# Optimization experiments

Measured on AMD Instinct MI355X. Metric: run time of the kernel, lower is better.

The kernel has to match this reference:

```python
import jax, jax.numpy as jnp
import numpy as np

L = 16            # clip_len
STRIDES = (2, 2)
RADII = (0.15, 0.3)
NSAMPLES = (16, 32)
EPS = 1e-5
NEG_SLOPE = 0.2


def _fps(xyz, npoint):
    # furthest point sampling, xyz: (N, 3) -> (npoint,) int32 indices, start at 0
    N = xyz.shape[0]
    def step(carry, _):
        mind, last = carry
        d = jnp.sum((xyz - xyz[last]) ** 2, axis=-1)
        mind = jnp.minimum(mind, d)
        nxt = jnp.argmax(mind).astype(jnp.int32)
        return (mind, nxt), nxt
    _, rest = jax.lax.scan(step, (jnp.full((N,), 1e10, xyz.dtype), jnp.int32(0)), None, length=npoint - 1)
    return jnp.concatenate([jnp.zeros((1,), jnp.int32), rest])


def _shift_point(xyz, batch, N):
    # torch.roll(points, -1, dims=1) over the temporal axis, with last-frame extrapolation fix
    p = xyz.reshape(batch // L, L, N, 3)
    s = jnp.roll(p, -1, axis=1)
    shift_mean = jnp.mean(s[:, :-1] - p[:, :-1], axis=1)   # (Bc, N, 3)
    s = s.at[:, -1].set(p[:, -1] + shift_mean)
    return s.reshape(batch, N, 3)


def _conv_bn_lrelu(x, w, g, b):
    # 1x1 Conv2d (no bias) + GroupBN (per-channel over all other dims) + LeakyReLU(0.2)
    y = jnp.einsum('oc,bcnk->bonk', w, x)
    mu = jnp.mean(y, axis=(0, 2, 3), keepdims=True)
    var = jnp.var(y, axis=(0, 2, 3), keepdims=True)
    y = (y - mu) * jax.lax.rsqrt(var + EPS) * g[None, :, None, None] + b[None, :, None, None]
    return jnp.where(y > 0, y, NEG_SLOPE * y)


def _sa_module(xyz, features, stride, radius, nsample, layers):
    # xyz: (B, N, 3), features: (B, C, N)
    batch, N = xyz.shape[0], xyz.shape[1]
    q = _shift_point(xyz, batch, N)
    npoint = N // stride if stride > 1 else N
    if stride > 1:
        idx = jax.vmap(lambda p: _fps(p, npoint))(jax.lax.stop_gradient(q))  # (B, npoint)
        q = jax.vmap(lambda p, ix: p[ix])(q, idx)                            # (B, npoint, 3)
    # ball query: first `nsample` neighbors of each query within `radius`, padded with first hit
    d2 = jnp.sum((q[:, :, None, :] - xyz[:, None, :, :]) ** 2, axis=-1)      # (B, npoint, N)
    mask = d2 < radius * radius
    cand = jnp.where(mask, jnp.arange(N, dtype=jnp.int32)[None, None, :], N)
    srt = jnp.sort(cand, axis=-1)[..., :nsample]
    first = srt[..., :1]
    gidx = jnp.where(srt == N, first, srt)
    gidx = jnp.where(gidx == N, 0, gidx)                                     # fallback: no neighbor
    grouped_xyz = jax.vmap(lambda pts, ix: pts[ix])(xyz, gidx)               # (B, npoint, ns, 3)
    dp = (grouped_xyz - q[:, :, None, :]) / radius                           # normalize_dp
    dist = jnp.linalg.norm(dp, axis=-1)                                      # (B, npoint, ns) -> 4th grouped channel
    feats = jnp.swapaxes(features, 1, 2)                                     # (B, N, C)
    grouped_f = jax.vmap(lambda f, ix: f[ix])(feats, gidx)                   # (B, npoint, ns, C)
    x = jnp.concatenate([dp, grouped_f], axis=-1)                            # (B, npoint, ns, 3 + C)
    x = jnp.transpose(x, (0, 3, 1, 2))                                       # (B, 3 + C, npoint, ns)
    for (w, g, b) in layers:
        x = _conv_bn_lrelu(x, w, g, b)
    gate = jax.nn.sigmoid(dist)[:, None, :, :]                               # sigmoid(points[:, -1:])
    out = jnp.max(gate * x, axis=-1)                                         # (B, Cout, npoint)
    return q, out


def _forward(xyz, w1a, g1a, b1a, w1b, g1b, b1b, w2a, g2a, b2a, w2b, g2b, b2b):
    features = jnp.swapaxes(xyz, 1, 2)                                       # features default = xyz^T
    q1, f1 = _sa_module(xyz, features, STRIDES[0], RADII[0], NSAMPLES[0],
                        [(w1a, g1a, b1a), (w1b, g1b, b1b)])
    q2, f2 = _sa_module(q1, f1, STRIDES[1], RADII[1], NSAMPLES[1],
                        [(w2a, g2a, b2a), (w2b, g2b, b2b)])
    return f2                                                                # (32, 256, 128)


def setup_inputs() -> dict:
    key = jax.random.key(0)
    ks = jax.random.split(key, 5)
    B, N = 32, 512   # B = 2 clips * clip_len 16
    xyz = jax.random.uniform(ks[0], (B, N, 3), jnp.float32)
    def w(k, o, i):
        return jax.random.normal(k, (o, i), jnp.float32) / np.sqrt(i).astype(np.float32)
    return {
        'xyz': xyz,
        'w1a': w(ks[1], 64, 6),    'g1a': jnp.ones(64),  'b1a': jnp.zeros(64),
        'w1b': w(ks[2], 128, 64),  'g1b': jnp.ones(128), 'b1b': jnp.zeros(128),
        'w2a': w(ks[3], 128, 131), 'g2a': jnp.ones(128), 'b2a': jnp.zeros(128),
        'w2b': w(ks[4], 256, 128), 'g2b': jnp.ones(256), 'b2b': jnp.zeros(256),
    }


def reference(xyz, w1a, g1a, b1a, w1b, g1b, b1b, w2a, g2a, b2a, w2b, g2b, b2b):
    return _forward(xyz, w1a, g1a, b1a, w1b, g1b, b1b, w2a, g2a, b2a, w2b, g2b, b2b)
```

## Files before the change

### kernel.cpp

```cpp
#include <hip/hip_runtime.h>
#include <hip/hip_bf16.h>
#include <math.h>


#define BATCH 32
#define MCOLS 131072
#define CGRID 2048

typedef __attribute__((ext_vector_type(8))) short short8;
typedef __attribute__((ext_vector_type(4))) short short4v;
typedef __attribute__((ext_vector_type(4))) float f32x4;

__device__ __forceinline__ float b2f(short s) {
    return __uint_as_float(((unsigned)(unsigned short)s) << 16);
}
__device__ __forceinline__ short f2b(float f) {
    __hip_bfloat16 h = __float2bfloat16(f);
    return (short)__builtin_bit_cast(unsigned short, h);
}
__device__ __forceinline__ float dpp_row16_sum(float v) {
    int x;
    x = __builtin_amdgcn_update_dpp(0, __float_as_int(v), 0x111, 0xf, 0xf, true);
    v += __int_as_float(x);
    x = __builtin_amdgcn_update_dpp(0, __float_as_int(v), 0x112, 0xf, 0xf, true);
    v += __int_as_float(x);
    x = __builtin_amdgcn_update_dpp(0, __float_as_int(v), 0x114, 0xf, 0xf, true);
    v += __int_as_float(x);
    x = __builtin_amdgcn_update_dpp(0, __float_as_int(v), 0x118, 0xf, 0xf, true);
    v += __int_as_float(x);
    return v;
}
template<int C>
__device__ __forceinline__ float dpp_max(float v) {
    int x = __builtin_amdgcn_update_dpp(0, __float_as_int(v), C, 0xf, 0xf, true);
    return fmaxf(v, __int_as_float(x));
}
__device__ __forceinline__ float readlane_f(float v, int lane) {
    return __int_as_float(__builtin_amdgcn_readlane(__float_as_int(v), lane));
}

__device__ __forceinline__ void prep_elem(const float* __restrict__ w, int O, int C,
                                          int CK, short* __restrict__ hi,
                                          short* __restrict__ lo, int t) {
    if (t >= O * CK) return;
    int o = t / CK, c = t % CK;
    float f = (c < C) ? w[o * C + c] : 0.f;
    short h = f2b(f);
    float fh = b2f(h);
    int NT = O >> 4;
    int ot = o >> 4, l15 = o & 15;
    int kc = c >> 5, quad = (c & 31) >> 3, j = c & 7;
    size_t idx = (((size_t)kc * NT + ot) * 64 + quad * 16 + l15) * 8 + j;
    hi[idx] = h;
    lo[idx] = f2b(f - fh);
}

__device__ __forceinline__ void shift_elem(const float* __restrict__ xyz,
                                           float* __restrict__ qout, int t, int N) {
    int c = t % 3;
    int n = (t / 3) % N;
    int b = t / (3 * N);
    int l = b & 15;
    float v;
    if (l < 15) {
        v = xyz[((size_t)(b + 1) * N + n) * 3 + c];
    } else {
        int g0 = b - 15;
        float acc = 0.f;
        for (int i = 0; i < 15; ++i) {
            float d = __fsub_rn(xyz[((size_t)(g0 + i + 1) * N + n) * 3 + c],
                                xyz[((size_t)(g0 + i) * N + n) * 3 + c]);
            acc = __fadd_rn(acc, d);
        }
        v = __fadd_rn(xyz[((size_t)b * N + n) * 3 + c], __fdiv_rn(acc, 15.f));
    }
    qout[t] = v;
}

__global__ __launch_bounds__(256) void setup_kernel(
        const float* __restrict__ w1a, const float* __restrict__ w1b,
        const float* __restrict__ w2a, const float* __restrict__ w2b,
        const float* __restrict__ xyz, float* __restrict__ qs1,
        short* w1aH, short* w1aL, short* w1bH, short* w1bL,
        short* w2aH, short* w2aL, short* w2bH, short* w2bL) {
    int bid = blockIdx.x;
    int tid = threadIdx.x;
    if (bid < 8)        prep_elem(w1a, 64, 6, 32,    w1aH, w1aL, bid * 256 + tid);
    else if (bid < 40)  prep_elem(w1b, 128, 64, 64,  w1bH, w1bL, (bid - 8) * 256 + tid);
    else if (bid < 120) prep_elem(w2a, 128, 131, 160, w2aH, w2aL, (bid - 40) * 256 + tid);
    else if (bid < 248) prep_elem(w2b, 256, 128, 128, w2bH, w2bL, (bid - 120) * 256 + tid);
    else {
        int t = (bid - 248) * 256 + tid;
        if (t < BATCH * 512 * 3) shift_elem(xyz, qs1, t, 512);
    }
}

template<int N, int NPOINT>
__device__ __forceinline__ void fps_spine(const float4* __restrict__ qp,
                                          int* __restrict__ sel, int lane) {
    constexpr int P = N / 64;
    float px[P], py[P], pz[P], mind[P];
#pragma unroll
    for (int p = 0; p < P; ++p) {
        float4 v = qp[lane * P + p];
        px[p] = v.x; py[p] = v.y; pz[p] = v.z;
        mind[p] = 1e10f;
    }
    float4 L0 = qp[0];
    float lx = L0.x, ly = L0.y, lz = L0.z;
    for (int s = 1; s < NPOINT; ++s) {
        float mn[P];
#pragma unroll
        for (int p = 0; p < P; ++p) {
            float dx = __fsub_rn(px[p], lx);
            float dy = __fsub_rn(py[p], ly);
            float dz = __fsub_rn(pz[p], lz);
            float d = __fadd_rn(__fadd_rn(__fmul_rn(dx, dx), __fmul_rn(dy, dy)),
                                __fmul_rn(dz, dz));
            float m2 = fminf(mind[p], d);
            mind[p] = m2;
            mn[p] = m2;
        }
        float t[P];
#pragma unroll
        for (int p = 0; p < P; ++p) t[p] = mn[p];
#pragma unroll
        for (int w = P / 2; w >= 1; w >>= 1)
#pragma unroll
            for (int p = 0; p < w; ++p) t[p] = fmaxf(t[p], t[p + w]);
        float local = t[0];
        float m = local;
        m = dpp_max<0x111>(m);
        m = dpp_max<0x112>(m);
        m = dpp_max<0x114>(m);
        m = dpp_max<0x118>(m);
        m = dpp_max<0x142>(m);
        m = dpp_max<0x143>(m);
        float maxd = readlane_f(m, 63);
        int enc = P - 1;
        float bx = px[P - 1], by = py[P - 1], bz = pz[P - 1];
#pragma unroll
        for (int p = P - 2; p >= 0; --p) {
            bool e = (mn[p] == local);
            enc = e ? p : enc;
            bx = e ? px[p] : bx;
            by = e ? py[p] : by;
            bz = e ? pz[p] : bz;
        }
        unsigned long long msk = __ballot(local == maxd);
        int winner = (int)__builtin_ctzll(msk);
        int last = winner * P + __builtin_amdgcn_readlane(enc, winner);
        lx = readlane_f(bx, winner);
        ly = readlane_f(by, winner);
        lz = readlane_f(bz, winner);
        if (lane == 0) sel[s] = last;
    }
}

template<int N, int NPOINT>
__global__ __launch_bounds__(64) void fps_kernel(const float* __restrict__ q,
                                                 float* __restrict__ qsel) {
    int b = blockIdx.x;
    int lane = threadIdx.x;
    __shared__ float4 qp[N];
    __shared__ int sel[NPOINT];
    const float* qb = q + (size_t)b * N * 3;
    for (int j = lane; j < N; j += 64)
        qp[j] = make_float4(qb[j * 3 + 0], qb[j * 3 + 1], qb[j * 3 + 2], 0.f);
    if (lane == 0) sel[0] = 0;
    __syncthreads();
    fps_spine<N, NPOINT>(qp, sel, lane);
    __syncthreads();
    for (int i = lane; i < NPOINT; i += 64) {
        float4 Pt = qp[sel[i]];
        size_t o = ((size_t)b * NPOINT + i) * 3;
        qsel[o + 0] = Pt.x;
        qsel[o + 1] = Pt.y;
        qsel[o + 2] = Pt.z;
    }
}

__device__ void fps256_body(const float* __restrict__ q, float* __restrict__ qsel,
                            int b, char* smem) {
    constexpr int N = 256, NPOINT = 128;
    float4* qp = (float4*)smem;
    int* sel = (int*)(smem + N * 16);
    int tid = threadIdx.x;
    const float* qb = q + (size_t)b * N * 3;
    for (int j = tid; j < N; j += 256)
        qp[j] = make_float4(qb[j * 3 + 0], qb[j * 3 + 1], qb[j * 3 + 2], 0.f);
    if (tid == 0) sel[0] = 0;
    __syncthreads();
    if (tid < 64) fps_spine<N, NPOINT>(qp, sel, tid);
    __syncthreads();
    for (int i = tid; i < NPOINT; i += 256) {
        float4 Pt = qp[sel[i]];
        size_t o = ((size_t)b * NPOINT + i) * 3;
        qsel[o + 0] = Pt.x;
        qsel[o + 1] = Pt.y;
        qsel[o + 2] = Pt.z;
    }
}

template<int N, int NPOINT, int NS, int CF, int CK>
__global__ __launch_bounds__(256) void ballq_kernel(
        const float* __restrict__ xyz,
        const float* __restrict__ qpts,
        const float* __restrict__ feats,
        float r2, float radius,
        short* __restrict__ X, float* __restrict__ gate) {
    static_assert((NS & (NS - 1)) == 0, "NS pow2");
    static_assert(CK % 8 == 0, "CK mult of 8");
    int lane = threadIdx.x & 63;
    int wib = threadIdx.x >> 6;
    int wid = blockIdx.x * 4 + wib;
    int b = wid / NPOINT;
    int i = wid % NPOINT;
    const float* qp = qpts + ((size_t)b * NPOINT + i) * 3;
    float qx = qp[0], qy = qp[1], qz = qp[2];
    __shared__ int gsh[4][NS];
    int* gidx = gsh[wib];
    int taken = 0, first = 0;
    bool any = false;
#pragma unroll
    for (int base = 0; base < N; base += 64) {
        int j = base + lane;
        const float* p = xyz + ((size_t)b * N + j) * 3;
        float dx = __fsub_rn(qx, p[0]);
        float dy = __fsub_rn(qy, p[1]);
        float dz = __fsub_rn(qz, p[2]);
        float d2 = __fadd_rn(__fadd_rn(__fmul_rn(dx, dx), __fmul_rn(dy, dy)),
                             __fmul_rn(dz, dz));
        bool in = d2 < r2;
        unsigned long long mk = __ballot(in);
        if (!any && mk) { first = base + __builtin_ctzll(mk); any = true; }
        int cb = __builtin_popcountll(mk & ((1ull << lane) - 1ull));
        int slot = taken + cb;
        if (in && slot < NS) gidx[slot] = j;
        taken += (int)__builtin_popcountll(mk);
    }
    if (taken < NS) {
        for (int s = taken + lane; s < NS; s += 64) gidx[s] = any ? first : 0;
    }
    __syncthreads();
    int m0 = (b * NPOINT + i) * NS;
    if (lane < NS) {
        int g = gidx[lane];
        const float* p = xyz + ((size_t)b * N + g) * 3;
        float dx = (p[0] - qx) / radius;
        float dy = (p[1] - qy) / radius;
        float dz = (p[2] - qz) / radius;
        float dist = sqrtf(dx * dx + dy * dy + dz * dz);
        gate[m0 + lane] = 1.f / (1.f + expf(-dist));
    }
    for (int e8 = lane * 8; e8 < NS * CK; e8 += 64 * 8) {
        int s = e8 / CK;
        int c0 = e8 % CK;
        int g = gidx[s];
        const float* frow = feats + (size_t)(b * N + g) * CF;
        const float* prow = xyz + ((size_t)b * N + g) * 3;
        short8 v8;
#pragma unroll
        for (int ii = 0; ii < 8; ++ii) {
            int c = c0 + ii;
            float v;
            if (c < 3) {
                float qc = (c == 0) ? qx : ((c == 1) ? qy : qz);
                v = (prow[c] - qc) / radius;
            } else if (c < 3 + CF) {
                v = frow[c - 3];
            } else {
                v = 0.f;
            }
            v8[ii] = f2b(v);
        }
        *(short8*)(X + (size_t)(m0 + s) * CK + c0) = v8;
    }
}

template<int CK, int O, bool AFF, bool FUSE>
__global__ __launch_bounds__(256, 3) void mfma_conv(
        const short* __restrict__ X, const short* __restrict__ Whi,
        const short* __restrict__ Wlo, const float* __restrict__ ss,
        short* __restrict__ Y, float* __restrict__ pS, float* __restrict__ pS2,
        const float* __restrict__ qs2, float* __restrict__ q2c) {
    constexpr int KC = CK / 32;
    constexpr int NT = O / 16;
    constexpr int OW = NT / 4;
    constexpr int LR = CK + 8;
    constexpr int CB = CK / 8;
    __shared__ __align__(16) short xs[64 * LR];
    __shared__ __align__(16) short wh[NT * 512];
    __shared__ __align__(16) short wl[NT * 512];
    __shared__ float ssl[AFF ? 2 * CK : 2];
    __shared__ float sblk[O], s2blk[O];
    static_assert(!FUSE || 64 * LR * 2 >= 256 * 16 + 128 * 4, "fps LDS fits in xs");
    if constexpr (FUSE) {
        if (blockIdx.x >= CGRID) {
            fps256_body(qs2, q2c, (int)blockIdx.x - CGRID, (char*)xs);
            return;
        }
    }
    int tid = threadIdx.x;
    int m0 = blockIdx.x * 64;

    if constexpr (AFF) {
        for (int i = tid; i < 2 * CK; i += 256) ssl[i] = ss[i];
        __syncthreads();
    }
    for (int idx = tid; idx < 64 * CB; idx += 256) {
        int r = idx / CB;
        int col = (idx % CB) * 8;
        short8 v = *(const short8*)(X + (size_t)(m0 + r) * CK + col);
        if constexpr (AFF) {
#pragma unroll
            for (int i = 0; i < 8; ++i) {
                float f = b2f(v[i]);
                f = fmaf(f, ssl[col + i], ssl[CK + col + i]);
                f = f > 0.f ? f : 0.2f * f;
                v[i] = f2b(f);
            }
        }
        *(short8*)(xs + r * LR + col) = v;
    }

    int lane = tid & 63;
    int wave = tid >> 6;
    int l15 = lane & 15;
    int quad = lane >> 4;
    int obase = wave * OW * 16;

    f32x4 acc[4][OW];
#pragma unroll
    for (int mt = 0; mt < 4; ++mt)
#pragma unroll
        for (int ot = 0; ot < OW; ++ot) acc[mt][ot] = (f32x4){0.f, 0.f, 0.f, 0.f};

    for (int kc = 0; kc < KC; ++kc) {
        __syncthreads();
        {
            const short8* gH = (const short8*)Whi + (size_t)kc * NT * 64;
            const short8* gL = (const short8*)Wlo + (size_t)kc * NT * 64;
            short8* lH = (short8*)wh;
            short8* lL = (short8*)wl;
            for (int i = tid; i < NT * 64; i += 256) { lH[i] = gH[i]; lL[i] = gL[i]; }
        }
        __syncthreads();
        short8 bf[4];
#pragma unroll
        for (int mt = 0; mt < 4; ++mt)
            bf[mt] = *(const short8*)(xs + (mt * 16 + l15) * LR + kc * 32 + quad * 8);
#pragma unroll
        for (int ot = 0; ot < OW; ++ot) {
            short8 ah = ((const short8*)wh)[(wave * OW + ot) * 64 + lane];
            short8 al = ((const short8*)wl)[(wave * OW + ot) * 64 + lane];
#pragma unroll
            for (int mt = 0; mt < 4; ++mt) {
                acc[mt][ot] = __builtin_amdgcn_mfma_f32_16x16x32_bf16(ah, bf[mt], acc[mt][ot], 0, 0, 0);
                acc[mt][ot] = __builtin_amdgcn_mfma_f32_16x16x32_bf16(al, bf[mt], acc[mt][ot], 0, 0, 0);
            }
        }
    }

#pragma unroll
    for (int mt = 0; mt < 4; ++mt) {
        size_t ybase = (size_t)(m0 + mt * 16 + l15) * O + obase + quad * 4;
#pragma unroll
        for (int ot = 0; ot < OW; ++ot) {
            short4v pk;
#pragma unroll
            for (int r4 = 0; r4 < 4; ++r4) pk[r4] = f2b(acc[mt][ot][r4]);
            *(short4v*)(Y + ybase + ot * 16) = pk;
        }
    }
#pragma unroll
    for (int ot = 0; ot < OW; ++ot) {
#pragma unroll
        for (int r4 = 0; r4 < 4; ++r4) {
            float s = 0.f, s2 = 0.f;
#pragma unroll
            for (int mt = 0; mt < 4; ++mt) {
                float v = acc[mt][ot][r4];
                s += v;
                s2 = fmaf(v, v, s2);
            }
            s = dpp_row16_sum(s);
            s2 = dpp_row16_sum(s2);
            if (l15 == 15) {
                int o = obase + ot * 16 + quad * 4 + r4;
                sblk[o] = s;
                s2blk[o] = s2;
            }
        }
    }
    __syncthreads();
    for (int o = tid; o < O; o += 256) {
        pS [(size_t)o * CGRID + blockIdx.x] = sblk[o];
        pS2[(size_t)o * CGRID + blockIdx.x] = s2blk[o];
    }
}

template<int O>
__global__ __launch_bounds__(256) void stats_fin(
        const float* __restrict__ pS, const float* __restrict__ pS2,
        const float* __restrict__ gm, const float* __restrict__ bt,
        float* __restrict__ norm) {
    int o = blockIdx.x;
    float s = 0.f, s2 = 0.f;
    for (int p = threadIdx.x; p < CGRID; p += 256) {
        s += pS[(size_t)o * CGRID + p];
        s2 += pS2[(size_t)o * CGRID + p];
    }
#pragma unroll
    for (int off = 32; off >= 1; off >>= 1) {
        s  += __shfl_xor(s,  off, 64);
        s2 += __shfl_xor(s2, off, 64);
    }
    __shared__ float sh[8];
    int wid = threadIdx.x >> 6;
    if ((threadIdx.x & 63) == 0) { sh[wid] = s; sh[4 + wid] = s2; }
    __syncthreads();
    if (threadIdx.x == 0) {
        float S  = sh[0] + sh[1] + sh[2] + sh[3];
        float S2 = sh[4] + sh[5] + sh[6] + sh[7];
        const float invM = 1.f / (float)MCOLS;
        float mu = S * invM;
        float var = S2 * invM - mu * mu;
        float sc = gm[o] * rsqrtf(var + 1e-5f);
        norm[o] = sc;
        norm[O + o] = bt[o] - mu * sc;
    }
}

__global__ __launch_bounds__(256) void stats_fin64_shift2(
        const float* __restrict__ pS, const float* __restrict__ pS2,
        const float* __restrict__ gm, const float* __restrict__ bt,
        float* __restrict__ norm,
        const float* __restrict__ q1c, float* __restrict__ qs2) {
    constexpr int O = 64;
    if (blockIdx.x >= O) {
        int t = (int)(blockIdx.x - O) * 256 + threadIdx.x;
        if (t < BATCH * 256 * 3) shift_elem(q1c, qs2, t, 256);
        return;
    }
    int o = blockIdx.x;
    float s = 0.f, s2 = 0.f;
    for (int p = threadIdx.x; p < CGRID; p += 256) {
        s += pS[(size_t)o * CGRID + p];
        s2 += pS2[(size_t)o * CGRID + p];
    }
#pragma unroll
    for (int off = 32; off >= 1; off >>= 1) {
        s  += __shfl_xor(s,  off, 64);
        s2 += __shfl_xor(s2, off, 64);
    }
    __shared__ float sh[8];
    int wid = threadIdx.x >> 6;
    if ((threadIdx.x & 63) == 0) { sh[wid] = s; sh[4 + wid] = s2; }
    __syncthreads();
    if (threadIdx.x == 0) {
        float S  = sh[0] + sh[1] + sh[2] + sh[3];
        float S2 = sh[4] + sh[5] + sh[6] + sh[7];
        const float invM = 1.f / (float)MCOLS;
        float mu = S * invM;
        float var = S2 * invM - mu * mu;
        float sc = gm[o] * rsqrtf(var + 1e-5f);
        norm[o] = sc;
        norm[O + o] = bt[o] - mu * sc;
    }
}

template<int NS, int NPOINT, int O>
__global__ __launch_bounds__(256) void pool1_kernel(
        const short* __restrict__ Y, const float* __restrict__ norm,
        const float* __restrict__ gate, float* __restrict__ out) {
    int t = blockIdx.x * 256 + threadIdx.x;
    int o = t % O;
    int n = (t / O) % NPOINT;
    int b = t / (O * NPOINT);
    int m0 = (b * NPOINT + n) * NS;
    float sc = norm[o], sf = norm[O + o];
    float best = -INFINITY;
#pragma unroll
    for (int k = 0; k < NS; ++k) {
        float v = fmaf(b2f(Y[(size_t)(m0 + k) * O + o]), sc, sf);
        v = v > 0.f ? v : 0.2f * v;
        best = fmaxf(best, gate[m0 + k] * v);
    }
    out[t] = best;
}

__global__ __launch_bounds__(256) void pool2_kernel(
        const short* __restrict__ Y, const float* __restrict__ norm,
        const float* __restrict__ gate, float* __restrict__ out) {
    constexpr int NS = 32, NPOINT = 128, O = 256;
    int b  = blockIdx.x >> 3;
    int oc = (blockIdx.x >> 1) & 3;
    int nc = blockIdx.x & 1;
    __shared__ float trans[64][65];
    int tid = threadIdx.x;
    for (int w = 0; w < 16; ++w) {
        int idx = w * 256 + tid;
        int o_l = idx & 63;
        int n_l = idx >> 6;
        int o = oc * 64 + o_l;
        int n = nc * 64 + n_l;
        int m0 = (b * NPOINT + n) * NS;
        float sc = norm[o], sf = norm[O + o];
        float best = -INFINITY;
#pragma unroll
        for (int k = 0; k < NS; ++k) {
            float v = fmaf(b2f(Y[(size_t)(m0 + k) * O + o]), sc, sf);
            v = v > 0.f ? v : 0.2f * v;
            best = fmaxf(best, gate[m0 + k] * v);
        }
        trans[o_l][n_l] = best;
    }
    __syncthreads();
    for (int w = 0; w < 16; ++w) {
        int idx = w * 256 + tid;
        int o_l = idx >> 6;
        int n_l = idx & 63;
        out[((size_t)b * O + oc * 64 + o_l) * NPOINT + nc * 64 + n_l] = trans[o_l][n_l];
    }
}

extern "C" void kernel_launch(void* const* d_in, const int* in_sizes, int n_in,
                              void* d_out, int out_size, void* d_ws, size_t ws_size,
                              hipStream_t stream) {
    const float* xyz = (const float*)d_in[0];
    const float* w1a = (const float*)d_in[1];
    const float* g1a = (const float*)d_in[2];
    const float* b1a = (const float*)d_in[3];
    const float* w1b = (const float*)d_in[4];
    const float* g1b = (const float*)d_in[5];
    const float* b1b = (const float*)d_in[6];
    const float* w2a = (const float*)d_in[7];
    const float* g2a = (const float*)d_in[8];
    const float* b2a = (const float*)d_in[9];
    const float* w2b = (const float*)d_in[10];
    const float* g2b = (const float*)d_in[11];
    const float* b2b = (const float*)d_in[12];

    char* ws = (char*)d_ws;
    constexpr size_t OFF_Q1C   = 0;
    constexpr size_t OFF_GATE1 = 98304;
    constexpr size_t OFF_Q2C   = 622592;
    constexpr size_t OFF_GATE2 = 671744;
    constexpr size_t OFF_NORM  = 1196032;
    constexpr size_t OFF_W     = 1204224;
    constexpr size_t OFF_PS    = 1499136;
    constexpr size_t OFF_PS2   = 3596288;
    constexpr size_t OFF_A     = 5693440;
    constexpr size_t OFF_B     = 39247872;
    constexpr size_t OFF_F1    = OFF_B + 41943040;
    constexpr size_t OFF_QS2   = 106356736;

    float* q1c   = (float*)(ws + OFF_Q1C);
    float* gate1 = (float*)(ws + OFF_GATE1);
    float* q2c   = (float*)(ws + OFF_Q2C);
    float* gate2 = (float*)(ws + OFF_GATE2);
    float* n1a   = (float*)(ws + OFF_NORM);
    float* n1b   = (float*)(ws + OFF_NORM + 512);
    float* n2a   = (float*)(ws + OFF_NORM + 1536);
    float* n2b   = (float*)(ws + OFF_NORM + 2560);
    short* w1aH  = (short*)(ws + OFF_W);
    short* w1aL  = w1aH + 2048;
    short* w1bH  = w1aL + 2048;
    short* w1bL  = w1bH + 8192;
    short* w2aH  = w1bL + 8192;
    short* w2aL  = w2aH + 20480;
    short* w2bH  = w2aL + 20480;
    short* w2bL  = w2bH + 32768;
    float* pS    = (float*)(ws + OFF_PS);
    float* pS2   = (float*)(ws + OFF_PS2);
    float* qs2   = (float*)(ws + OFF_QS2);

    char* A = ws + OFF_A;
    char* B = ws + OFF_B;
    short* X1  = (short*)A;
    short* Y1a = (short*)B;
    short* Y1b = (short*)A;
    short* X2  = (short*)B;
    short* Y2a = (short*)A;
    short* Y2b = (short*)B;
    float* qs1 = (float*)B;
    float* f1  = (float*)(ws + OFF_F1);

    const float r2_1 = (float)(0.15 * 0.15);
    const float r2_2 = (float)(0.3 * 0.3);

    setup_kernel<<<440, 256, 0, stream>>>(w1a, w1b, w2a, w2b, xyz, qs1,
                                          w1aH, w1aL, w1bH, w1bL,
                                          w2aH, w2aL, w2bH, w2bL);

    fps_kernel<512, 256><<<32, 64, 0, stream>>>(qs1, q1c);
    ballq_kernel<512, 256, 16, 3, 32><<<2048, 256, 0, stream>>>(
        xyz, q1c, xyz, r2_1, 0.15f, X1, gate1);
    mfma_conv<32, 64, false, false><<<CGRID, 256, 0, stream>>>(
        X1, w1aH, w1aL, nullptr, Y1a, pS, pS2, nullptr, nullptr);
    stats_fin64_shift2<<<160, 256, 0, stream>>>(pS, pS2, g1a, b1a, n1a, q1c, qs2);
    mfma_conv<64, 128, true, true><<<CGRID + 32, 256, 0, stream>>>(
        Y1a, w1bH, w1bL, n1a, Y1b, pS, pS2, qs2, q2c);
    stats_fin<128><<<128, 256, 0, stream>>>(pS, pS2, g1b, b1b, n1b);
    pool1_kernel<16, 256, 128><<<4096, 256, 0, stream>>>(Y1b, n1b, gate1, f1);

    ballq_kernel<256, 128, 32, 128, 160><<<1024, 256, 0, stream>>>(
        q1c, q2c, f1, r2_2, 0.3f, X2, gate2);
    mfma_conv<160, 128, false, false><<<CGRID, 256, 0, stream>>>(
        X2, w2aH, w2aL, nullptr, Y2a, pS, pS2, nullptr, nullptr);
    stats_fin<128><<<128, 256, 0, stream>>>(pS, pS2, g2a, b2a, n2a);
    mfma_conv<128, 256, true, false><<<CGRID, 256, 0, stream>>>(
        Y2a, w2bH, w2bL, n2a, Y2b, pS, pS2, nullptr, nullptr);
    stats_fin<256><<<256, 256, 0, stream>>>(pS, pS2, g2b, b2b, n2b);
    pool2_kernel<<<256, 256, 0, stream>>>(Y2b, n2b, gate2, (float*)d_out);
}
```

Before: 381.7 us.

## Fuse first ball query with first 6-channel conv and partial stats

```diff
diff --git a/kernel.cpp b/kernel.cpp
--- a/kernel.cpp
+++ b/kernel.cpp
@@ -78,19 +78,18 @@
 }
 
 __global__ __launch_bounds__(256) void setup_kernel(
-        const float* __restrict__ w1a, const float* __restrict__ w1b,
-        const float* __restrict__ w2a, const float* __restrict__ w2b,
+        const float* __restrict__ w1b, const float* __restrict__ w2a,
+        const float* __restrict__ w2b,
         const float* __restrict__ xyz, float* __restrict__ qs1,
-        short* w1aH, short* w1aL, short* w1bH, short* w1bL,
+        short* w1bH, short* w1bL,
         short* w2aH, short* w2aL, short* w2bH, short* w2bL) {
     int bid = blockIdx.x;
     int tid = threadIdx.x;
-    if (bid < 8)        prep_elem(w1a, 64, 6, 32,    w1aH, w1aL, bid * 256 + tid);
-    else if (bid < 40)  prep_elem(w1b, 128, 64, 64,  w1bH, w1bL, (bid - 8) * 256 + tid);
-    else if (bid < 120) prep_elem(w2a, 128, 131, 160, w2aH, w2aL, (bid - 40) * 256 + tid);
-    else if (bid < 248) prep_elem(w2b, 256, 128, 128, w2bH, w2bL, (bid - 120) * 256 + tid);
+    if (bid < 32)       prep_elem(w1b, 128, 64, 64,   w1bH, w1bL, bid * 256 + tid);
+    else if (bid < 112) prep_elem(w2a, 128, 131, 160, w2aH, w2aL, (bid - 32) * 256 + tid);
+    else if (bid < 240) prep_elem(w2b, 256, 128, 128, w2bH, w2bL, (bid - 112) * 256 + tid);
     else {
-        int t = (bid - 248) * 256 + tid;
+        int t = (bid - 240) * 256 + tid;
         if (t < BATCH * 512 * 3) shift_elem(xyz, qs1, t, 512);
     }
 }
@@ -199,6 +198,93 @@
         qsel[o + 0] = Pt.x;
         qsel[o + 1] = Pt.y;
         qsel[o + 2] = Pt.z;
+    }
+}
+
+template<int N, int NPOINT, int NS>
+__global__ __launch_bounds__(256) void ballq1_conv(
+        const float* __restrict__ xyz,
+        const float* __restrict__ qpts,
+        const float* __restrict__ w1a,
+        float r2, float radius,
+        short* __restrict__ Y, float* __restrict__ gate,
+        float* __restrict__ pS, float* __restrict__ pS2) {
+    static_assert((NS & (NS - 1)) == 0, "NS pow2");
+    constexpr int O = 64;
+    int tid = threadIdx.x;
+    int lane = tid & 63;
+    int wib = tid >> 6;
+    int wid = blockIdx.x * 4 + wib;
+    int b = wid / NPOINT;
+    int i = wid % NPOINT;
+    const float* qp = qpts + ((size_t)b * NPOINT + i) * 3;
+    float qx = qp[0], qy = qp[1], qz = qp[2];
+    __shared__ int gsh[4][NS];
+    __shared__ float xsh[4][NS][6];
+    __shared__ float wsh[O * 6];
+    __shared__ float sblk[4][O], s2blk[4][O];
+    for (int k = tid; k < O * 6; k += 256) wsh[k] = w1a[k];
+    int* gidx = gsh[wib];
+    int taken = 0, first = 0;
+    bool any = false;
+#pragma unroll
+    for (int base = 0; base < N; base += 64) {
+        int j = base + lane;
+        const float* p = xyz + ((size_t)b * N + j) * 3;
+        float dx = __fsub_rn(qx, p[0]);
+        float dy = __fsub_rn(qy, p[1]);
+        float dz = __fsub_rn(qz, p[2]);
+        float d2 = __fadd_rn(__fadd_rn(__fmul_rn(dx, dx), __fmul_rn(dy, dy)),
+                             __fmul_rn(dz, dz));
+        bool in = d2 < r2;
+        unsigned long long mk = __ballot(in);
+        if (!any && mk) { first = base + __builtin_ctzll(mk); any = true; }
+        int cb = __builtin_popcountll(mk & ((1ull << lane) - 1ull));
+        int slot = taken + cb;
+        if (in && slot < NS) gidx[slot] = j;
+        taken += (int)__builtin_popcountll(mk);
+    }
+    if (taken < NS) {
+        for (int s = taken + lane; s < NS; s += 64) gidx[s] = any ? first : 0;
+    }
+    __syncthreads();
+    int m0 = wid * NS;
+    if (lane < NS) {
+        int g = gidx[lane];
+        const float* p = xyz + ((size_t)b * N + g) * 3;
+        float dx = (p[0] - qx) / radius;
+        float dy = (p[1] - qy) / radius;
+        float dz = (p[2] - qz) / radius;
+        float dist = sqrtf(dx * dx + dy * dy + dz * dz);
+        gate[m0 + lane] = 1.f / (1.f + expf(-dist));
+        xsh[wib][lane][0] = dx;
+        xsh[wib][lane][1] = dy;
+        xsh[wib][lane][2] = dz;
+        xsh[wib][lane][3] = p[0];
+        xsh[wib][lane][4] = p[1];
+        xsh[wib][lane][5] = p[2];
+    }
+    __syncthreads();
+    float w0 = wsh[lane * 6 + 0], w1 = wsh[lane * 6 + 1], w2 = wsh[lane * 6 + 2];
+    float w3 = wsh[lane * 6 + 3], w4 = wsh[lane * 6 + 4], w5 = wsh[lane * 6 + 5];
+    float sum = 0.f, sum2 = 0.f;
+#pragma unroll
+    for (int s = 0; s < NS; ++s) {
+        const float* x = xsh[wib][s];
+        float y = fmaf(x[5], w5, fmaf(x[4], w4, fmaf(x[3], w3,
+                  fmaf(x[2], w2, fmaf(x[1], w1, x[0] * w0)))));
+        Y[(size_t)(m0 + s) * O + lane] = f2b(y);
+        sum += y;
+        sum2 = fmaf(y, y, sum2);
+    }
+    sblk[wib][lane] = sum;
+    s2blk[wib][lane] = sum2;
+    __syncthreads();
+    if (tid < O) {
+        float S  = sblk[0][tid] + sblk[1][tid] + sblk[2][tid] + sblk[3][tid];
+        float S2 = s2blk[0][tid] + s2blk[1][tid] + s2blk[2][tid] + s2blk[3][tid];
+        pS [(size_t)tid * CGRID + blockIdx.x] = S;
+        pS2[(size_t)tid * CGRID + blockIdx.x] = S2;
     }
 }
 
@@ -564,9 +650,7 @@
     float* n1b   = (float*)(ws + OFF_NORM + 512);
     float* n2a   = (float*)(ws + OFF_NORM + 1536);
     float* n2b   = (float*)(ws + OFF_NORM + 2560);
-    short* w1aH  = (short*)(ws + OFF_W);
-    short* w1aL  = w1aH + 2048;
-    short* w1bH  = w1aL + 2048;
+    short* w1bH  = (short*)(ws + OFF_W);
     short* w1bL  = w1bH + 8192;
     short* w2aH  = w1bL + 8192;
     short* w2aL  = w2aH + 20480;
@@ -578,7 +662,6 @@
 
     char* A = ws + OFF_A;
     char* B = ws + OFF_B;
-    short* X1  = (short*)A;
     short* Y1a = (short*)B;
     short* Y1b = (short*)A;
     short* X2  = (short*)B;
@@ -590,15 +673,12 @@
     const float r2_1 = (float)(0.15 * 0.15);
     const float r2_2 = (float)(0.3 * 0.3);
 
-    setup_kernel<<<440, 256, 0, stream>>>(w1a, w1b, w2a, w2b, xyz, qs1,
-                                          w1aH, w1aL, w1bH, w1bL,
-                                          w2aH, w2aL, w2bH, w2bL);
+    setup_kernel<<<432, 256, 0, stream>>>(w1b, w2a, w2b, xyz, qs1,
+                                          w1bH, w1bL, w2aH, w2aL, w2bH, w2bL);
 
     fps_kernel<512, 256><<<32, 64, 0, stream>>>(qs1, q1c);
-    ballq_kernel<512, 256, 16, 3, 32><<<2048, 256, 0, stream>>>(
-        xyz, q1c, xyz, r2_1, 0.15f, X1, gate1);
-    mfma_conv<32, 64, false, false><<<CGRID, 256, 0, stream>>>(
-        X1, w1aH, w1aL, nullptr, Y1a, pS, pS2, nullptr, nullptr);
+    ballq1_conv<512, 256, 16><<<2048, 256, 0, stream>>>(
+        xyz, q1c, w1a, r2_1, 0.15f, Y1a, gate1, pS, pS2);
     stats_fin64_shift2<<<160, 256, 0, stream>>>(pS, pS2, g1a, b1a, n1a, q1c, qs2);
     mfma_conv<64, 128, true, true><<<CGRID + 32, 256, 0, stream>>>(
         Y1a, w1bH, w1bL, n1a, Y1b, pS, pS2, qs2, q2c);
```

Measured after the change: 372.8 us (median of 2 runs). -2.3%, faster.
